# Performance work log

Hardware: AMD Instinct MI355X
Metric: run time of the kernel (lower is better)

The kernel has to match this reference:

```python
import math
import jax, jax.numpy as jnp
import numpy as np

L, H, K, NH, V, DFF = 6, 512, 512, 8, 64, 1024
B, T, S = 8, 512, 512
PAD = 0


def _ln(x, g, b, eps=1e-5):
    m = jnp.mean(x, -1, keepdims=True)
    v = jnp.mean((x - m) ** 2, -1, keepdims=True)
    return (x - m) * jax.lax.rsqrt(v + eps) * g + b


def _mha(Q, Kin, Vin, mask, wq, bq, wk, bk, wv, bv, wo, bo, g, b):
    # weights stored [in, out]
    B_, Tq, Hd = Q.shape
    dk = wq.shape[1] // NH
    dv = wv.shape[1] // NH
    q = (Q @ wq + bq).reshape(B_, Tq, NH, dk).transpose(0, 2, 1, 3)
    k = (Kin @ wk + bk).reshape(B_, -1, NH, dk).transpose(0, 2, 1, 3)
    v = (Vin @ wv + bv).reshape(B_, -1, NH, dv).transpose(0, 2, 1, 3)
    scores = jnp.einsum('bhqd,bhkd->bhqk', q, k) / jnp.sqrt(jnp.float32(dk))
    scores = jnp.where(mask[:, None, :, :], jnp.float32(-1e9), scores)
    attn = jax.nn.softmax(scores, axis=-1)
    ctx = jnp.einsum('bhqk,bhkd->bhqd', attn, v).transpose(0, 2, 1, 3).reshape(B_, Tq, Hd)
    return _ln(ctx @ wo + bo + Q, g, b)


def _pe(t, d):
    pos = jnp.arange(t, dtype=jnp.float32)[:, None]
    div = jnp.exp(jnp.arange(0, d, 2, dtype=jnp.float32) * (-math.log(10000.0) / d))
    pe = jnp.zeros((t, d), jnp.float32)
    pe = pe.at[:, 0::2].set(jnp.sin(pos * div)).at[:, 1::2].set(jnp.cos(pos * div))
    return pe


def setup_inputs() -> dict:
    key = jax.random.key(0)
    ks = iter(jax.random.split(key, 40))
    nrm = lambda shape, s=0.02: jax.random.normal(next(ks), shape, jnp.float32) * s
    inp = {
        'smiles_index': jax.random.randint(next(ks), (B, T), 0, V, dtype=jnp.int32),
        'enc_outputs': jax.random.normal(next(ks), (B, S, H), jnp.float32),
        'enc_pad_mask': jnp.zeros((B, 1, S), bool),
        'tgt_len': T,
        'mol_emb': nrm((V, H), 1.0).at[PAD].set(0.0),  # padding_idx=0 row zeroed
        # self-attn stacks [L, ...]
        'sa_wq': nrm((L, H, K)), 'sa_bq': jnp.zeros((L, K)),
        'sa_wk': nrm((L, H, K)), 'sa_bk': jnp.zeros((L, K)),
        'sa_wv': nrm((L, H, H)), 'sa_bv': jnp.zeros((L, H)),
        'sa_wo': nrm((L, H, H)), 'sa_bo': jnp.zeros((L, H)),
        'ln1_g': jnp.ones((L, H)), 'ln1_b': jnp.zeros((L, H)),
        # cross-attn stacks
        'ea_wq': nrm((L, H, K)), 'ea_bq': jnp.zeros((L, K)),
        'ea_wk': nrm((L, H, K)), 'ea_bk': jnp.zeros((L, K)),
        'ea_wv': nrm((L, H, H)), 'ea_bv': jnp.zeros((L, H)),
        'ea_wo': nrm((L, H, H)), 'ea_bo': jnp.zeros((L, H)),
        'ln2_g': jnp.ones((L, H)), 'ln2_b': jnp.zeros((L, H)),
        # conv1x1 FFN == per-position linear
        'c1_w': nrm((L, H, DFF)), 'c1_b': jnp.zeros((L, DFF)),
        'c2_w': nrm((L, DFF, H)), 'c2_b': jnp.zeros((L, H)),
        'ln3_g': jnp.ones((L, H)), 'ln3_b': jnp.zeros((L, H)),
    }
    return inp


def reference(smiles_index, enc_outputs, enc_pad_mask, tgt_len, mol_emb,
              sa_wq, sa_bq, sa_wk, sa_bk, sa_wv, sa_bv, sa_wo, sa_bo, ln1_g, ln1_b,
              ea_wq, ea_bq, ea_wk, ea_bk, ea_wv, ea_bv, ea_wo, ea_bo, ln2_g, ln2_b,
              c1_w, c1_b, c2_w, c2_b, ln3_g, ln3_b):
    b, t = smiles_index.shape
    s = enc_outputs.shape[1]
    # embeddings + sinusoidal positional encoding (dropout is identity in eval)
    x = mol_emb[smiles_index] + _pe(t, mol_emb.shape[1])[None]
    # masks: pad (key == pad_id) OR causal upper-triangular
    pad = (smiles_index == PAD)[:, None, :]                 # [B,1,T] -> broadcast over queries
    causal = jnp.triu(jnp.ones((t, t), bool), 1)[None]      # [1,T,T]
    self_mask = pad | causal                                # [B,T,T]
    enc_mask = jnp.broadcast_to(enc_pad_mask, (b, t, s))    # [B,T,S]
    for l in range(L):
        x = _mha(x, x, x, self_mask,
                 sa_wq[l], sa_bq[l], sa_wk[l], sa_bk[l], sa_wv[l], sa_bv[l],
                 sa_wo[l], sa_bo[l], ln1_g[l], ln1_b[l])
        x = _mha(x, enc_outputs, enc_outputs, enc_mask,
                 ea_wq[l], ea_bq[l], ea_wk[l], ea_bk[l], ea_wv[l], ea_bv[l],
                 ea_wo[l], ea_bo[l], ln2_g[l], ln2_b[l])
        h = jax.nn.relu(x @ c1_w[l] + c1_b[l])
        y = h @ c2_w[l] + c2_b[l]
        x = _ln(y + x, ln3_g[l], ln3_b[l])
    return x
```

## Files before the change

kernel.cpp:

```cpp
#include <hip/hip_runtime.h>
#include <hip/hip_bf16.h>
#include <math.h>

#define NL   6
#define HD   512
#define NHD  8
#define DK   64
#define DFFN 1024
#define NB   8
#define TT   512
#define MROWS (NB*TT)
#define SQC  262144

typedef __hip_bfloat16 bf16;
typedef __attribute__((ext_vector_type(8))) short short8v;
typedef __attribute__((ext_vector_type(4))) short short4v;
typedef __attribute__((ext_vector_type(4))) float f32x4;

__device__ __forceinline__ float wave_sum(float v) {
#pragma unroll
  for (int off = 32; off; off >>= 1) v += __shfl_xor(v, off);
  return v;
}
__device__ __forceinline__ unsigned short f2bf(float x) {
  __hip_bfloat16 h = __float2bfloat16(x);
  return *reinterpret_cast<unsigned short*>(&h);
}
__device__ __forceinline__ float bf2f(unsigned short u) {
  return __uint_as_float(((unsigned)u) << 16);
}

struct Srcs8 { const float* s[8]; };
__global__ __launch_bounds__(256)
void wprep8_kernel(Srcs8 srcs, bf16* __restrict__ wt) {
  const int z = blockIdx.z;
  const int which = z & 7, l = z >> 3;
  const long long baseT[8] = {0, 0, 0, 18LL*SQC, 24LL*SQC, 30LL*SQC, 30LL*SQC, 42LL*SQC};
  const long long lstrT[8] = {3LL*SQC, 3LL*SQC, 3LL*SQC, SQC, SQC, 2LL*SQC, 2LL*SQC, SQC};
  const int rowOffT[8] = {0, 512, 1024, 0, 0, 0, 512, 0};

  __shared__ float t[32][33];
  const float* W = srcs.s[which] + (size_t)l * SQC;
  bf16* dst = wt + baseT[which] + (size_t)l * lstrT[which] + (size_t)rowOffT[which] * HD;
  const int n0 = blockIdx.x * 32, k0 = blockIdx.y * 32;
  const int tx = threadIdx.x & 31, ty = threadIdx.x >> 5;
#pragma unroll
  for (int j = 0; j < 4; ++j)
    t[ty + j * 8][tx] = W[(size_t)(k0 + ty + j * 8) * HD + n0 + tx];
  __syncthreads();
#pragma unroll
  for (int j = 0; j < 4; ++j)
    dst[(size_t)(n0 + ty + j * 8) * HD + k0 + tx] = __float2bfloat16(t[tx][ty + j * 8]);
}

__global__ __launch_bounds__(256)
void wprep_kernel(const float* __restrict__ W, bf16* __restrict__ Wt, int Kd, int Nd) {
  __shared__ float t[32][33];
  const size_t src = (size_t)blockIdx.z * Kd * Nd;
  const int n0 = blockIdx.x * 32, k0 = blockIdx.y * 32;
  const int tx = threadIdx.x & 31, ty = threadIdx.x >> 5;
#pragma unroll
  for (int j = 0; j < 4; ++j)
    t[ty + j * 8][tx] = W[src + (size_t)(k0 + ty + j * 8) * Nd + n0 + tx];
  __syncthreads();
#pragma unroll
  for (int j = 0; j < 4; ++j)
    Wt[src + (size_t)(n0 + ty + j * 8) * Kd + k0 + tx] = __float2bfloat16(t[tx][ty + j * 8]);
}

__global__ __launch_bounds__(256)
void bcat2_kernel(const float* __restrict__ b0, const float* __restrict__ b1,
                  const float* __restrict__ b2, const float* __restrict__ c0,
                  const float* __restrict__ c1, float* __restrict__ outS,
                  float* __restrict__ outKV) {
  const int l = blockIdx.x;
  if (blockIdx.y == 0) {
    for (int i = threadIdx.x; i < 1536; i += 256) {
      const int seg = i >> 9, off = i & 511;
      const float* src = seg == 0 ? b0 : (seg == 1 ? b1 : b2);
      outS[(size_t)l * 1536 + i] = src[(size_t)l * 512 + off];
    }
  } else {
    for (int i = threadIdx.x; i < 1024; i += 256) {
      const float* src = (i >> 9) == 0 ? c0 : c1;
      outKV[(size_t)l * 1024 + i] = src[(size_t)l * 512 + (i & 511)];
    }
  }
}

__global__ __launch_bounds__(256)
void cvtbf16_kernel(const float* __restrict__ in, unsigned short* __restrict__ out) {
  const int i = (blockIdx.x * 256 + threadIdx.x) * 4;
  float4 v = *(const float4*)(in + i);
  out[i + 0] = f2bf(v.x); out[i + 1] = f2bf(v.y);
  out[i + 2] = f2bf(v.z); out[i + 3] = f2bf(v.w);
}

__global__ __launch_bounds__(256)
void embed_pe_kernel(const int* __restrict__ idx, const float* __restrict__ emb,
                     float* __restrict__ x, unsigned short* __restrict__ xb) {
  const int row = blockIdx.x;
  const int t = row & (TT - 1);
  const int tok = idx[row];
  const float cdiv = -0.017988946009466842f;
#pragma unroll
  for (int e0 = 0; e0 < 2; ++e0) {
    const int e = threadIdx.x + e0 * 256;
    const float div = __expf((float)(e & ~1) * cdiv);
    const float ang = (float)t * div;
    const float pe = (e & 1) ? cosf(ang) : sinf(ang);
    const float v = emb[(size_t)tok * HD + e] + pe;
    x[(size_t)row * HD + e] = v;
    xb[(size_t)row * HD + e] = f2bf(v);
  }
}

__device__ __forceinline__ void gemm_compute(const char* As, const char* Bs,
                                             int wm, int wn, int lane,
                                             f32x4 (&acc)[2][2]) {
  const int rsw = (lane & 7) << 4;
  const int csel = (lane >> 4) * 16;
  short8v af[2][2], bfr[2][2];
#pragma unroll
  for (int m = 0; m < 2; ++m)
#pragma unroll
    for (int kk = 0; kk < 2; ++kk) {
      const int row = wm * 32 + m * 16 + (lane & 15);
      af[m][kk] = *(const short8v*)(As + row * 128 + ((kk * 64 + csel) ^ rsw));
    }
#pragma unroll
  for (int n = 0; n < 2; ++n)
#pragma unroll
    for (int kk = 0; kk < 2; ++kk) {
      const int row = wn * 32 + n * 16 + (lane & 15);
      bfr[n][kk] = *(const short8v*)(Bs + row * 128 + ((kk * 64 + csel) ^ rsw));
    }
#pragma unroll
  for (int m = 0; m < 2; ++m)
#pragma unroll
    for (int n = 0; n < 2; ++n) {
      acc[m][n] = __builtin_amdgcn_mfma_f32_16x16x32_bf16(af[m][0], bfr[n][0], acc[m][n], 0, 0, 0);
      acc[m][n] = __builtin_amdgcn_mfma_f32_16x16x32_bf16(af[m][1], bfr[n][1], acc[m][n], 0, 0, 0);
    }
}

template<int OUT_BF16, int RELU, int ADDRES>
__device__ __forceinline__
void mgemm_body(const bf16* __restrict__ A, const bf16* __restrict__ Bt,
                const float* __restrict__ bias, const float* __restrict__ res,
                float* __restrict__ Cf, unsigned short* __restrict__ Cb,
                int N, int K, int m0, int n0, char* As, char* Bs) {
  const int tid = threadIdx.x;
  const int w = tid >> 6, lane = tid & 63;
  const int wm = w >> 1, wn = w & 1;

  const int sr = w * 16 + (lane >> 3);
  const int scol = (lane & 7) * 16;
  const int swc = scol ^ ((sr & 7) << 4);
  const bf16* ga0 = A + (size_t)(m0 + sr) * K + (scol >> 1);
  const bf16* ga1 = A + (size_t)(m0 + sr + 8) * K + (scol >> 1);
  const bf16* gb0 = Bt + (size_t)(n0 + sr) * K + (scol >> 1);
  const bf16* gb1 = Bt + (size_t)(n0 + sr + 8) * K + (scol >> 1);
  char* la0 = As + sr * 128 + swc;
  char* la1 = As + (sr + 8) * 128 + swc;
  char* lb0 = Bs + sr * 128 + swc;
  char* lb1 = Bs + (sr + 8) * 128 + swc;

  f32x4 acc[2][2] = {};

  short8v ra0 = *(const short8v*)ga0, ra1 = *(const short8v*)ga1;
  short8v rb0 = *(const short8v*)gb0, rb1 = *(const short8v*)gb1;
  short8v sa0, sa1, sb0, sb1;

  for (int k0 = 0; k0 < K; k0 += 128) {
    __syncthreads();
    *(short8v*)la0 = ra0; *(short8v*)la1 = ra1;
    *(short8v*)lb0 = rb0; *(short8v*)lb1 = rb1;
    __syncthreads();
    sa0 = *(const short8v*)(ga0 + k0 + 64); sa1 = *(const short8v*)(ga1 + k0 + 64);
    sb0 = *(const short8v*)(gb0 + k0 + 64); sb1 = *(const short8v*)(gb1 + k0 + 64);
    gemm_compute(As, Bs, wm, wn, lane, acc);
    __syncthreads();
    *(short8v*)la0 = sa0; *(short8v*)la1 = sa1;
    *(short8v*)lb0 = sb0; *(short8v*)lb1 = sb1;
    __syncthreads();
    if (k0 + 128 < K) {
      ra0 = *(const short8v*)(ga0 + k0 + 128); ra1 = *(const short8v*)(ga1 + k0 + 128);
      rb0 = *(const short8v*)(gb0 + k0 + 128); rb1 = *(const short8v*)(gb1 + k0 + 128);
    }
    gemm_compute(As, Bs, wm, wn, lane, acc);
  }

  const int crow = (lane >> 4) * 4;
  const int ccol = lane & 15;
#pragma unroll
  for (int m = 0; m < 2; ++m)
#pragma unroll
    for (int n = 0; n < 2; ++n) {
      const int gr = m0 + wm * 32 + m * 16 + crow;
      const int gc = n0 + wn * 32 + n * 16 + ccol;
      const float bs = bias[gc];
#pragma unroll
      for (int r = 0; r < 4; ++r) {
        float v = acc[m][n][r] + bs;
        if (RELU) v = fmaxf(v, 0.f);
        if (ADDRES) v += res[(size_t)(gr + r) * N + gc];
        if (OUT_BF16) Cb[(size_t)(gr + r) * N + gc] = f2bf(v);
        else          Cf[(size_t)(gr + r) * N + gc] = v;
      }
    }
}

template<int OUT_BF16, int RELU, int ADDRES>
__global__ __launch_bounds__(256)
void mgemm_kernel(const bf16* __restrict__ A, const bf16* __restrict__ Bt,
                  const float* __restrict__ bias, const float* __restrict__ res,
                  float* __restrict__ Cf, unsigned short* __restrict__ Cb,
                  int N, int K) {
  __shared__ __attribute__((aligned(16))) char As[64 * 128];
  __shared__ __attribute__((aligned(16))) char Bs[64 * 128];
  mgemm_body<OUT_BF16, RELU, ADDRES>(A, Bt, bias, res, Cf, Cb, N, K,
                                     blockIdx.x * 64, blockIdx.y * 64, As, Bs);
}

__global__ __launch_bounds__(256)
void mgemm_eakv_kernel(const bf16* __restrict__ A, const bf16* __restrict__ BtBase,
                       const float* __restrict__ biasBase, unsigned short* __restrict__ CBase) {
  __shared__ __attribute__((aligned(16))) char As[64 * 128];
  __shared__ __attribute__((aligned(16))) char Bs[64 * 128];
  const int l = blockIdx.y >> 4, ny = blockIdx.y & 15;
  mgemm_body<1, 0, 0>(A, BtBase + (size_t)l * 2 * SQC, biasBase + (size_t)l * 1024,
                      nullptr, nullptr, CBase + (size_t)l * MROWS * 1024,
                      1024, 512, blockIdx.x * 64, ny * 64, As, Bs);
}

template<int CAUSAL>
__global__ __launch_bounds__(512)
void mattn_kernel(const unsigned short* __restrict__ q, const unsigned short* __restrict__ kgl,
                  const unsigned short* __restrict__ vgl, unsigned short* __restrict__ ctx,
                  const int* __restrict__ idx, const unsigned char* __restrict__ emask,
                  int qstride, int kvstride) {
  __shared__ __attribute__((aligned(16))) unsigned short kt[64 * 64];
  __shared__ __attribute__((aligned(16))) unsigned short vt[64 * 64];
  __shared__ __attribute__((aligned(16))) unsigned short pl[8][16 * 64];
  __shared__ float km[64];

  const int bh = blockIdx.x;
  const int b = bh >> 3, h = bh & 7;
  const int tid = threadIdx.x, w = tid >> 6, lane = tid & 63;
  const int l4 = lane & 15, g = lane >> 4;

  int qb_w;
  if (CAUSAL) {
    const int strip = (w < 4) ? blockIdx.y : 7 - blockIdx.y;
    qb_w = strip * 64 + (w & 3) * 16;
  } else {
    qb_w = blockIdx.y * 128 + w * 16;
  }
  const int kvEnd = CAUSAL ? (8 - blockIdx.y) * 64 : TT;

  const unsigned short* qp = q + (size_t)(b * TT + qb_w + l4) * qstride + h * DK + g * 8;
  short8v aq0 = *(const short8v*)qp;
  short8v aq1 = *(const short8v*)(qp + 32);

  const int sr_k = tid >> 3, sc8 = tid & 7;
  const unsigned short* kbp = kgl + (size_t)(b * TT + sr_k) * kvstride + h * DK + sc8 * 8;
  const int k2 = (tid & 31) * 2, d4 = (tid >> 5) * 4;
  const unsigned short* vbp0 = vgl + (size_t)(b * TT + k2) * kvstride + h * DK + d4;
  const unsigned short* vbp1 = vbp0 + kvstride;

  short8v rk = *(const short8v*)kbp;
  short4v rv0 = *(const short4v*)vbp0;
  short4v rv1 = *(const short4v*)vbp1;
  float mreg = 0.f;
  if (tid < 64) {
    const int kp = b * TT + tid;
    mreg = (CAUSAL ? (idx[kp] == 0) : (emask[kp] != 0)) ? -1e9f : 0.f;
  }

  float m_r[4], l_r[4];
  f32x4 acc_o[4];
#pragma unroll
  for (int r = 0; r < 4; ++r) { m_r[r] = -1e30f; l_r[r] = 0.f; }
#pragma unroll
  for (int f = 0; f < 4; ++f) acc_o[f] = (f32x4){0.f, 0.f, 0.f, 0.f};

  for (int kt0 = 0; kt0 < kvEnd; kt0 += 64) {
    __syncthreads();
    if (tid < 64) km[tid] = mreg;
    *(short8v*)((char*)kt + sr_k * 128 + ((sc8 * 16) ^ ((sr_k & 7) << 4))) = rk;
#pragma unroll
    for (int j = 0; j < 4; ++j) {
      const int d = d4 + j;
      const unsigned pk = ((unsigned)(unsigned short)rv0[j]) | (((unsigned)(unsigned short)rv1[j]) << 16);
      *(unsigned*)((char*)vt + d * 128 + ((k2 * 2) ^ ((d & 7) << 4))) = pk;
    }
    __syncthreads();

    if (kt0 + 64 < kvEnd) {
      const size_t off = (size_t)(kt0 + 64) * kvstride;
      rk = *(const short8v*)(kbp + off);
      rv0 = *(const short4v*)(vbp0 + off);
      rv1 = *(const short4v*)(vbp1 + off);
      if (tid < 64) {
        const int kp = b * TT + kt0 + 64 + tid;
        mreg = (CAUSAL ? (idx[kp] == 0) : (emask[kp] != 0)) ? -1e9f : 0.f;
      }
    }

    if (!(CAUSAL && kt0 > qb_w + 15)) {
      const bool diag = CAUSAL && (kt0 + 64 > qb_w);

      f32x4 s4[4];
      __builtin_amdgcn_s_setprio(1);
#pragma unroll
      for (int f = 0; f < 4; ++f) {
        const int krow = f * 16 + l4;
        const int sw = (krow & 7) << 4;
        short8v bk0 = *(const short8v*)((const char*)kt + krow * 128 + ((g * 16) ^ sw));
        short8v bk1 = *(const short8v*)((const char*)kt + krow * 128 + ((64 + g * 16) ^ sw));
        f32x4 a = {};
        a = __builtin_amdgcn_mfma_f32_16x16x32_bf16(aq0, bk0, a, 0, 0, 0);
        a = __builtin_amdgcn_mfma_f32_16x16x32_bf16(aq1, bk1, a, 0, 0, 0);
        s4[f] = a;
      }
      __builtin_amdgcn_s_setprio(0);

      float kmb[4];
#pragma unroll
      for (int f = 0; f < 4; ++f) kmb[f] = km[f * 16 + l4];

      float sc_r[4];
#pragma unroll
      for (int r = 0; r < 4; ++r) {
        const int qpos = qb_w + g * 4 + r;
        float sf[4];
#pragma unroll
        for (int f = 0; f < 4; ++f) sf[f] = fmaf(s4[f][r], 0.125f, kmb[f]);
        if (diag) {
#pragma unroll
          for (int f = 0; f < 4; ++f) {
            const int kpos = kt0 + f * 16 + l4;
            sf[f] = (kpos > qpos) ? -1e9f : sf[f];
          }
        }
        float mx = fmaxf(fmaxf(sf[0], sf[1]), fmaxf(sf[2], sf[3]));
#pragma unroll
        for (int off = 8; off; off >>= 1) mx = fmaxf(mx, __shfl_xor(mx, off));
        const float mn = fmaxf(m_r[r], mx);
        const float sc = __expf(m_r[r] - mn);
        m_r[r] = mn;
        sc_r[r] = sc;
        float ps = 0.f;
        const int prow = g * 4 + r;
        const int psw = (prow & 7) << 4;
#pragma unroll
        for (int f = 0; f < 4; ++f) {
          const float p = __expf(sf[f] - mn);
          ps += p;
          *(unsigned short*)((char*)pl[w] + prow * 128 + ((f * 32 + l4 * 2) ^ psw)) = f2bf(p);
        }
#pragma unroll
        for (int off = 8; off; off >>= 1) ps += __shfl_xor(ps, off);
        l_r[r] = l_r[r] * sc + ps;
      }

#pragma unroll
      for (int f = 0; f < 4; ++f)
#pragma unroll
        for (int r = 0; r < 4; ++r) acc_o[f][r] *= sc_r[r];

      const int asw = (l4 & 7) << 4;
      short8v pa0 = *(const short8v*)((const char*)pl[w] + l4 * 128 + ((g * 16) ^ asw));
      short8v pa1 = *(const short8v*)((const char*)pl[w] + l4 * 128 + ((g * 16 + 64) ^ asw));
      __builtin_amdgcn_s_setprio(1);
#pragma unroll
      for (int f = 0; f < 4; ++f) {
        const int drow = f * 16 + l4;
        const int sw = (drow & 7) << 4;
        short8v vb0 = *(const short8v*)((const char*)vt + drow * 128 + ((g * 16) ^ sw));
        short8v vb1 = *(const short8v*)((const char*)vt + drow * 128 + ((g * 16 + 64) ^ sw));
        acc_o[f] = __builtin_amdgcn_mfma_f32_16x16x32_bf16(pa0, vb0, acc_o[f], 0, 0, 0);
        acc_o[f] = __builtin_amdgcn_mfma_f32_16x16x32_bf16(pa1, vb1, acc_o[f], 0, 0, 0);
      }
      __builtin_amdgcn_s_setprio(0);
    }
  }

  float rl[4];
#pragma unroll
  for (int r = 0; r < 4; ++r) rl[r] = 1.f / l_r[r];
#pragma unroll
  for (int f = 0; f < 4; ++f)
#pragma unroll
    for (int r = 0; r < 4; ++r) {
      const int row = qb_w + g * 4 + r;
      const int col = h * DK + f * 16 + l4;
      ctx[(size_t)(b * TT + row) * HD + col] = f2bf(acc_o[f][r] * rl[r]);
    }
}

__global__ __launch_bounds__(256)
void ln2_kernel(const unsigned short* __restrict__ v, float* __restrict__ out,
                unsigned short* __restrict__ outb,
                const float* __restrict__ g, const float* __restrict__ bta) {
  const int row = blockIdx.x;
  const int tid = threadIdx.x;
  const int w = tid >> 6, lane = tid & 63;
  const size_t ro = (size_t)row * HD;

  float v0 = bf2f(v[ro + tid]);
  float v1 = bf2f(v[ro + tid + 256]);

  __shared__ float red[4];
  float s = wave_sum(v0 + v1);
  if (lane == 0) red[w] = s;
  __syncthreads();
  const float mean = (red[0] + red[1] + red[2] + red[3]) * (1.f / HD);
  __syncthreads();

  const float d0 = v0 - mean, d1 = v1 - mean;
  float qv = wave_sum(d0 * d0 + d1 * d1);
  if (lane == 0) red[w] = qv;
  __syncthreads();
  const float var = (red[0] + red[1] + red[2] + red[3]) * (1.f / HD);
  const float rstd = rsqrtf(var + 1e-5f);

  const float o0 = d0 * rstd * g[tid] + bta[tid];
  const float o1 = d1 * rstd * g[tid + 256] + bta[tid + 256];
  out[ro + tid] = o0;
  out[ro + tid + 256] = o1;
  outb[ro + tid] = f2bf(o0);
  outb[ro + tid + 256] = f2bf(o1);
}

extern "C" void kernel_launch(void* const* d_in, const int* in_sizes, int n_in,
                              void* d_out, int out_size, void* d_ws, size_t ws_size,
                              hipStream_t stream) {
  const int* idx = (const int*)d_in[0];
  const float* enc = (const float*)d_in[1];
  const unsigned char* emask = (const unsigned char*)d_in[2];
  const float* emb = (const float*)d_in[4];
  const float* sa_wq = (const float*)d_in[5];
  const float* sa_bq = (const float*)d_in[6];
  const float* sa_wk = (const float*)d_in[7];
  const float* sa_bk = (const float*)d_in[8];
  const float* sa_wv = (const float*)d_in[9];
  const float* sa_bv = (const float*)d_in[10];
  const float* sa_wo = (const float*)d_in[11];
  const float* sa_bo = (const float*)d_in[12];
  const float* ln1g = (const float*)d_in[13];
  const float* ln1b = (const float*)d_in[14];
  const float* ea_wq = (const float*)d_in[15];
  const float* ea_bq = (const float*)d_in[16];
  const float* ea_wk = (const float*)d_in[17];
  const float* ea_bk = (const float*)d_in[18];
  const float* ea_wv = (const float*)d_in[19];
  const float* ea_bv = (const float*)d_in[20];
  const float* ea_wo = (const float*)d_in[21];
  const float* ea_bo = (const float*)d_in[22];
  const float* ln2g = (const float*)d_in[23];
  const float* ln2b = (const float*)d_in[24];
  const float* c1w = (const float*)d_in[25];
  const float* c1b = (const float*)d_in[26];
  const float* c2w = (const float*)d_in[27];
  const float* c2b = (const float*)d_in[28];
  const float* ln3g = (const float*)d_in[29];
  const float* ln3b = (const float*)d_in[30];

  const size_t MH = (size_t)MROWS * HD;
  const size_t SQ = (size_t)SQC;
  char* ws = (char*)d_ws;
  float*          x    = (float*)(ws + 0);
  unsigned short* xb   = (unsigned short*)(ws + (8u << 20));
  unsigned short* qkvb = (unsigned short*)(ws + (12u << 20));
  unsigned short* qcb  = (unsigned short*)(ws + (24u << 20));
  unsigned short* cxb  = (unsigned short*)(ws + (28u << 20));
  unsigned short* ybb  = (unsigned short*)(ws + (32u << 20));
  unsigned short* encb = (unsigned short*)(ws + (36u << 20));
  bf16*           wt   = (bf16*)(ws + (40u << 20));
  float*          bcS  = (float*)(ws + (78u << 20));
  float*          bcKV = (float*)(ws + (79u << 20));
  unsigned short* kvb6 = (unsigned short*)(ws + (80u << 20));
  unsigned short* hb   = qkvb;

  bf16* t_saqkv = wt;
  bf16* t_sao   = wt + 18 * SQ;
  bf16* t_eaq   = wt + 24 * SQ;
  bf16* t_eakv  = wt + 30 * SQ;
  bf16* t_eao   = wt + 42 * SQ;
  bf16* t_c1    = wt + 48 * SQ;
  bf16* t_c2    = wt + 60 * SQ;

  const dim3 blk(256);
  const dim3 blk512(512);
  const dim3 gQKV(MROWS / 64, 1536 / 64);
  const dim3 g1024(MROWS / 64, 1024 / 64);
  const dim3 g512(MROWS / 64, 512 / 64);
  const dim3 gEAKV(MROWS / 64, 96);
  const dim3 attng(NB * NHD, 4);

  Srcs8 s8;
  s8.s[0] = sa_wq; s8.s[1] = sa_wk; s8.s[2] = sa_wv; s8.s[3] = sa_wo;
  s8.s[4] = ea_wq; s8.s[5] = ea_wk; s8.s[6] = ea_wv; s8.s[7] = ea_wo;
  wprep8_kernel<<<dim3(16, 16, 48), blk, 0, stream>>>(s8, wt);
  wprep_kernel<<<dim3(32, 16, NL), blk, 0, stream>>>(c1w, t_c1, HD, DFFN);
  wprep_kernel<<<dim3(16, 32, NL), blk, 0, stream>>>(c2w, t_c2, DFFN, HD);
  bcat2_kernel<<<dim3(NL, 2), blk, 0, stream>>>(sa_bq, sa_bk, sa_bv, ea_bk, ea_bv, bcS, bcKV);
  cvtbf16_kernel<<<MH / 1024, blk, 0, stream>>>(enc, encb);
  mgemm_eakv_kernel<<<gEAKV, blk, 0, stream>>>((const bf16*)encb, t_eakv, bcKV, kvb6);

  embed_pe_kernel<<<MROWS, blk, 0, stream>>>(idx, emb, x, xb);

  for (int l = 0; l < NL; ++l) {
    const size_t b512 = (size_t)l * HD;
    const size_t bFF = (size_t)l * DFFN;
    float* lnout = (l == NL - 1) ? (float*)d_out : x;
    unsigned short* kvl = kvb6 + (size_t)l * MROWS * 1024;

    mgemm_kernel<1, 0, 0><<<gQKV, blk, 0, stream>>>(
        (const bf16*)xb, t_saqkv + (size_t)l * 3 * SQ, bcS + (size_t)l * 1536,
        nullptr, nullptr, qkvb, 1536, HD);
    mattn_kernel<1><<<attng, blk512, 0, stream>>>(qkvb, qkvb + 512, qkvb + 1024, cxb,
                                                  idx, emask, 1536, 1536);
    mgemm_kernel<1, 0, 1><<<g512, blk, 0, stream>>>(
        (const bf16*)cxb, t_sao + (size_t)l * SQ, sa_bo + b512, x, nullptr, ybb, HD, HD);
    ln2_kernel<<<MROWS, blk, 0, stream>>>(ybb, x, xb, ln1g + b512, ln1b + b512);

    mgemm_kernel<1, 0, 0><<<g512, blk, 0, stream>>>(
        (const bf16*)xb, t_eaq + (size_t)l * SQ, ea_bq + b512, nullptr, nullptr, qcb, HD, HD);
    mattn_kernel<0><<<attng, blk512, 0, stream>>>(qcb, kvl, kvl + 512, cxb,
                                                  idx, emask, 512, 1024);
    mgemm_kernel<1, 0, 1><<<g512, blk, 0, stream>>>(
        (const bf16*)cxb, t_eao + (size_t)l * SQ, ea_bo + b512, x, nullptr, ybb, HD, HD);
    ln2_kernel<<<MROWS, blk, 0, stream>>>(ybb, x, xb, ln2g + b512, ln2b + b512);

    mgemm_kernel<1, 1, 0><<<g1024, blk, 0, stream>>>(
        (const bf16*)xb, t_c1 + (size_t)l * 2 * SQ, c1b + bFF, nullptr, nullptr, hb, DFFN, HD);
    mgemm_kernel<1, 0, 1><<<g512, blk, 0, stream>>>(
        (const bf16*)hb, t_c2 + (size_t)l * 2 * SQ, c2b + b512, x, nullptr, ybb, HD, DFFN);
    ln2_kernel<<<MROWS, blk, 0, stream>>>(ybb, lnout, xb, ln3g + b512, ln3b + b512);
  }
}
```

Baseline: 820.0 us.

## Use 128x128 tiles for cross-attn KV GEMM and one-wave-per-row LayerNorm

Rewrites the batched cross-attention K/V projection GEMM to compute 128x128 output tiles per block, with four waves each holding a 4x4 grid of MFMA accumulators and register-prefetched global loads. The larger tile raises arithmetic intensity and cuts redundant loads of A and B compared with the 64x64 shared body. The LayerNorm kernel is changed to handle one row per wave with vectorized 16-byte loads and stores and shuffle-only reductions, removing shared-memory barriers and launching a quarter as many blocks. In exchange, the GEMM uses more registers and shared memory per block, which may lower occupancy.

```diff
diff --git a/kernel.cpp b/kernel.cpp
--- a/kernel.cpp
+++ b/kernel.cpp
@@ -226,12 +226,81 @@
 __global__ __launch_bounds__(256)
 void mgemm_eakv_kernel(const bf16* __restrict__ A, const bf16* __restrict__ BtBase,
                        const float* __restrict__ biasBase, unsigned short* __restrict__ CBase) {
-  __shared__ __attribute__((aligned(16))) char As[64 * 128];
-  __shared__ __attribute__((aligned(16))) char Bs[64 * 128];
-  const int l = blockIdx.y >> 4, ny = blockIdx.y & 15;
-  mgemm_body<1, 0, 0>(A, BtBase + (size_t)l * 2 * SQC, biasBase + (size_t)l * 1024,
-                      nullptr, nullptr, CBase + (size_t)l * MROWS * 1024,
-                      1024, 512, blockIdx.x * 64, ny * 64, As, Bs);
+  __shared__ __attribute__((aligned(16))) char As[128 * 128];
+  __shared__ __attribute__((aligned(16))) char Bs[128 * 128];
+  const int l = blockIdx.y >> 3, ny = blockIdx.y & 7;
+  const bf16* Bt = BtBase + (size_t)l * 2 * SQC;
+  const float* bias = biasBase + (size_t)l * 1024;
+  unsigned short* C = CBase + (size_t)l * MROWS * 1024;
+  const int m0 = blockIdx.x * 128, n0 = ny * 128;
+  const int tid = threadIdx.x, w = tid >> 6, lane = tid & 63;
+  const int wm = w >> 1, wn = w & 1;
+  const int c8 = tid & 7, rg0 = tid >> 3;
+  const int K = 512;
+
+  const bf16* gA[4]; const bf16* gB[4];
+  char* lA[4]; char* lB[4];
+#pragma unroll
+  for (int j = 0; j < 4; ++j) {
+    const int r = rg0 + 32 * j;
+    gA[j] = A  + (size_t)(m0 + r) * K + c8 * 8;
+    gB[j] = Bt + (size_t)(n0 + r) * K + c8 * 8;
+    const int swz = (c8 * 16) ^ ((r & 7) << 4);
+    lA[j] = As + r * 128 + swz;
+    lB[j] = Bs + r * 128 + swz;
+  }
+
+  f32x4 acc[4][4] = {};
+  short8v rA[4], rB[4];
+#pragma unroll
+  for (int j = 0; j < 4; ++j) { rA[j] = *(const short8v*)gA[j]; rB[j] = *(const short8v*)gB[j]; }
+
+  const int l4 = lane & 15, g = lane >> 4;
+  for (int t = 0; t < 8; ++t) {
+    __syncthreads();
+#pragma unroll
+    for (int j = 0; j < 4; ++j) { *(short8v*)lA[j] = rA[j]; *(short8v*)lB[j] = rB[j]; }
+    __syncthreads();
+    if (t + 1 < 8) {
+#pragma unroll
+      for (int j = 0; j < 4; ++j) {
+        rA[j] = *(const short8v*)(gA[j] + (t + 1) * 64);
+        rB[j] = *(const short8v*)(gB[j] + (t + 1) * 64);
+      }
+    }
+#pragma unroll
+    for (int kk = 0; kk < 2; ++kk) {
+      short8v af[4], bv[4];
+#pragma unroll
+      for (int fm = 0; fm < 4; ++fm) {
+        const int row = wm * 64 + fm * 16 + l4;
+        af[fm] = *(const short8v*)(As + row * 128 + ((kk * 64 + g * 16) ^ ((row & 7) << 4)));
+      }
+#pragma unroll
+      for (int fn = 0; fn < 4; ++fn) {
+        const int row = wn * 64 + fn * 16 + l4;
+        bv[fn] = *(const short8v*)(Bs + row * 128 + ((kk * 64 + g * 16) ^ ((row & 7) << 4)));
+      }
+#pragma unroll
+      for (int fm = 0; fm < 4; ++fm)
+#pragma unroll
+        for (int fn = 0; fn < 4; ++fn)
+          acc[fm][fn] = __builtin_amdgcn_mfma_f32_16x16x32_bf16(af[fm], bv[fn], acc[fm][fn], 0, 0, 0);
+    }
+  }
+
+  const int crow = (lane >> 4) * 4, ccol = l4;
+#pragma unroll
+  for (int fm = 0; fm < 4; ++fm)
+#pragma unroll
+    for (int fn = 0; fn < 4; ++fn) {
+      const int gr = m0 + wm * 64 + fm * 16 + crow;
+      const int gc = n0 + wn * 64 + fn * 16 + ccol;
+      const float bs = bias[gc];
+#pragma unroll
+      for (int r = 0; r < 4; ++r)
+        C[(size_t)(gr + r) * 1024 + gc] = f2bf(acc[fm][fn][r] + bs);
+    }
 }
 
 template<int CAUSAL>
@@ -404,34 +473,44 @@
 void ln2_kernel(const unsigned short* __restrict__ v, float* __restrict__ out,
                 unsigned short* __restrict__ outb,
                 const float* __restrict__ g, const float* __restrict__ bta) {
-  const int row = blockIdx.x;
-  const int tid = threadIdx.x;
-  const int w = tid >> 6, lane = tid & 63;
-  const size_t ro = (size_t)row * HD;
-
-  float v0 = bf2f(v[ro + tid]);
-  float v1 = bf2f(v[ro + tid + 256]);
-
-  __shared__ float red[4];
-  float s = wave_sum(v0 + v1);
-  if (lane == 0) red[w] = s;
-  __syncthreads();
-  const float mean = (red[0] + red[1] + red[2] + red[3]) * (1.f / HD);
-  __syncthreads();
-
-  const float d0 = v0 - mean, d1 = v1 - mean;
-  float qv = wave_sum(d0 * d0 + d1 * d1);
-  if (lane == 0) red[w] = qv;
-  __syncthreads();
-  const float var = (red[0] + red[1] + red[2] + red[3]) * (1.f / HD);
-  const float rstd = rsqrtf(var + 1e-5f);
-
-  const float o0 = d0 * rstd * g[tid] + bta[tid];
-  const float o1 = d1 * rstd * g[tid + 256] + bta[tid + 256];
-  out[ro + tid] = o0;
-  out[ro + tid + 256] = o1;
-  outb[ro + tid] = f2bf(o0);
-  outb[ro + tid + 256] = f2bf(o1);
+  const int row = blockIdx.x * 4 + (threadIdx.x >> 6);
+  const int lane = threadIdx.x & 63;
+  const size_t ro = (size_t)row * HD + lane * 8;
+
+  short8v u = *(const short8v*)(v + ro);
+  float f[8];
+#pragma unroll
+  for (int j = 0; j < 8; ++j) f[j] = bf2f((unsigned short)u[j]);
+
+  float s = 0.f;
+#pragma unroll
+  for (int j = 0; j < 8; ++j) s += f[j];
+  s = wave_sum(s);
+  const float mean = s * (1.f / HD);
+
+  float qv = 0.f;
+#pragma unroll
+  for (int j = 0; j < 8; ++j) { const float d = f[j] - mean; qv += d * d; }
+  qv = wave_sum(qv);
+  const float rstd = rsqrtf(qv * (1.f / HD) + 1e-5f);
+
+  const float4 g0 = *(const float4*)(g + lane * 8);
+  const float4 g1 = *(const float4*)(g + lane * 8 + 4);
+  const float4 b0 = *(const float4*)(bta + lane * 8);
+  const float4 b1 = *(const float4*)(bta + lane * 8 + 4);
+  float gg[8] = {g0.x, g0.y, g0.z, g0.w, g1.x, g1.y, g1.z, g1.w};
+  float bb[8] = {b0.x, b0.y, b0.z, b0.w, b1.x, b1.y, b1.z, b1.w};
+
+  float o[8];
+  short8v ob;
+#pragma unroll
+  for (int j = 0; j < 8; ++j) {
+    o[j] = (f[j] - mean) * rstd * gg[j] + bb[j];
+    ob[j] = (short)f2bf(o[j]);
+  }
+  *(float4*)(out + ro) = (float4){o[0], o[1], o[2], o[3]};
+  *(float4*)(out + ro + 4) = (float4){o[4], o[5], o[6], o[7]};
+  *(short8v*)(outb + ro) = ob;
 }
 
 extern "C" void kernel_launch(void* const* d_in, const int* in_sizes, int n_in,
@@ -497,7 +576,8 @@
   const dim3 gQKV(MROWS / 64, 1536 / 64);
   const dim3 g1024(MROWS / 64, 1024 / 64);
   const dim3 g512(MROWS / 64, 512 / 64);
-  const dim3 gEAKV(MROWS / 64, 96);
+  const dim3 gEAKV(MROWS / 128, 48);
+  const dim3 gLN(MROWS / 4);
   const dim3 attng(NB * NHD, 4);
 
   Srcs8 s8;
@@ -525,7 +605,7 @@
                                                   idx, emask, 1536, 1536);
     mgemm_kernel<1, 0, 1><<<g512, blk, 0, stream>>>(
         (const bf16*)cxb, t_sao + (size_t)l * SQ, sa_bo + b512, x, nullptr, ybb, HD, HD);
-    ln2_kernel<<<MROWS, blk, 0, stream>>>(ybb, x, xb, ln1g + b512, ln1b + b512);
+    ln2_kernel<<<gLN, blk, 0, stream>>>(ybb, x, xb, ln1g + b512, ln1b + b512);
 
     mgemm_kernel<1, 0, 0><<<g512, blk, 0, stream>>>(
         (const bf16*)xb, t_eaq + (size_t)l * SQ, ea_bq + b512, nullptr, nullptr, qcb, HD, HD);
@@ -533,12 +613,12 @@
                                                   idx, emask, 512, 1024);
     mgemm_kernel<1, 0, 1><<<g512, blk, 0, stream>>>(
         (const bf16*)cxb, t_eao + (size_t)l * SQ, ea_bo + b512, x, nullptr, ybb, HD, HD);
-    ln2_kernel<<<MROWS, blk, 0, stream>>>(ybb, x, xb, ln2g + b512, ln2b + b512);
+    ln2_kernel<<<gLN, blk, 0, stream>>>(ybb, x, xb, ln2g + b512, ln2b + b512);
 
     mgemm_kernel<1, 1, 0><<<g1024, blk, 0, stream>>>(
         (const bf16*)xb, t_c1 + (size_t)l * 2 * SQ, c1b + bFF, nullptr, nullptr, hb, DFFN, HD);
     mgemm_kernel<1, 0, 1><<<g512, blk, 0, stream>>>(
         (const bf16*)hb, t_c2 + (size_t)l * 2 * SQ, c2b + b512, x, nullptr, ybb, HD, DFFN);
-    ln2_kernel<<<MROWS, blk, 0, stream>>>(ybb, lnout, xb, ln3g + b512, ln3b + b512);
-  }
-}
+    ln2_kernel<<<gLN, blk, 0, stream>>>(ybb, lnout, xb, ln3g + b512, ln3b + b512);
+  }
+}
```

Result: faster. 799.6 us (-2.5%).
